# Performance work log

Hardware: AMD Instinct MI355X
Metric: run time of the kernel (lower is better)

Reference implementation:

```python
import math
import jax, jax.numpy as jnp
import numpy as np

K = 4          # beats_per_bar
POS_DIM = 32   # fourier pos-embed dim


def setup_inputs() -> dict:
    key = jax.random.key(0)
    k1, k2, k3 = jax.random.split(key, 3)
    B, M, D = 8, 8192, 1024
    beat_emb = jax.random.normal(k1, (B, M, D), dtype=jnp.float32)
    W = jax.random.normal(k2, (D, D + POS_DIM), dtype=jnp.float32) * 0.02  # nn.Linear weight [out, in]
    b = jax.random.normal(k3, (D,), dtype=jnp.float32) * 0.02
    return {"beat_emb": beat_emb, "W": W, "b": b}


def _fourier_features(pos, dim):
    # pos: [Mb] in [0,1] -> [Mb, dim] (dim even, so no zero-pad branch needed)
    half = dim // 2
    freqs = jnp.exp(jnp.linspace(0.0, math.log(1000.0), half)).astype(pos.dtype)
    ang = pos[:, None] * freqs  # [Mb, half]
    return jnp.concatenate([jnp.sin(ang), jnp.cos(ang)], axis=-1)


def reference(beat_emb, W, b):
    B, M, D = beat_emb.shape
    Mb = (M + K - 1) // K
    pad = Mb * K - M
    x = jnp.pad(beat_emb, ((0, 0), (0, pad), (0, 0))) if pad else beat_emb
    # fused segment mean: [B, Mb, K, D] -> sum -> divide by actual segment length
    sums = x.reshape(B, Mb, K, D).sum(axis=2)
    counts = jnp.minimum(K, M - jnp.arange(Mb) * K).astype(beat_emb.dtype)  # [Mb]
    out = sums / counts[None, :, None]  # [B, Mb, D]
    # fourier positional features on normalized bar index (same for every batch row)
    idx = jnp.arange(Mb, dtype=beat_emb.dtype)
    pos = jnp.clip(idx / max(1, Mb - 1), 0.0, 1.0)
    ff = _fourier_features(pos, POS_DIM)                     # [Mb, POS_DIM]
    ff = jnp.broadcast_to(ff[None], (B, Mb, POS_DIM))
    h = jnp.concatenate([out, ff], axis=-1)                  # [B, Mb, D+POS_DIM]
    return jnp.einsum('bmi,oi->bmo', h, W) + b               # Linear: x @ W.T + b
```

## Files before the change

### kernel.cpp

```cpp
#include <hip/hip_runtime.h>
#include <math.h>
#include <stdint.h>
#include <stddef.h>

typedef short bf16x8 __attribute__((ext_vector_type(8)));
typedef short bf16x4 __attribute__((ext_vector_type(4)));
typedef float f32x4  __attribute__((ext_vector_type(4)));

#define BATCH   8
#define M_IN    8192
#define D_IN    1024
#define POSD    32
#define KD      1056
#define MBARS   2048
#define MROWS   16384
#define NOUT    1024

__device__ __forceinline__ short f2bf(float f) {
    unsigned u = __builtin_bit_cast(unsigned, f);
    u += 0x7fffu + ((u >> 16) & 1u);
    return (short)(u >> 16);
}

__device__ __forceinline__ void async_load16(const short* g, short* l) {
    __builtin_amdgcn_global_load_lds((__attribute__((address_space(1))) void*)g,
                                     (__attribute__((address_space(3))) void*)l,
                                     16, 0, 0);
}

__global__ __launch_bounds__(256) void wcast(const float* __restrict__ W,
                                             short* __restrict__ Wb) {
    int i = blockIdx.x * 256 + threadIdx.x;
    float4 v = ((const float4*)W)[i];
    bf16x4 o = { f2bf(v.x), f2bf(v.y), f2bf(v.z), f2bf(v.w) };
    ((bf16x4*)Wb)[i] = o;
}

__global__ __launch_bounds__(256) void pool_ff(const float* __restrict__ x,
                                               short* __restrict__ h) {
    const int row = blockIdx.x;
    const int t   = threadIdx.x;
    const float4* src = (const float4*)(x + (size_t)row * 4096);
    float4 s0 = src[t];
    float4 s1 = src[t + 256];
    float4 s2 = src[t + 512];
    float4 s3 = src[t + 768];
    float mx = (s0.x + s1.x + s2.x + s3.x) * 0.25f;
    float my = (s0.y + s1.y + s2.y + s3.y) * 0.25f;
    float mz = (s0.z + s1.z + s2.z + s3.z) * 0.25f;
    float mw = (s0.w + s1.w + s2.w + s3.w) * 0.25f;
    bf16x4 o = { f2bf(mx), f2bf(my), f2bf(mz), f2bf(mw) };
    *(bf16x4*)(h + (size_t)row * KD + t * 4) = o;

    if (t < POSD) {
        const int mb = row & (MBARS - 1);
        float pos = (float)mb * (1.0f / (float)(MBARS - 1));
        float fr  = expf((float)(t & 15) * (6.907755278982137f / 15.0f));
        float ang = pos * fr;
        float v   = (t < 16) ? sinf(ang) : cosf(ang);
        h[(size_t)row * KD + D_IN + t] = f2bf(v);
    }
}

__global__ __launch_bounds__(256) void gemm_bt(const short* __restrict__ A,
                                               const short* __restrict__ B,
                                               const float* __restrict__ bias,
                                               float* __restrict__ C) {
    __shared__ short As[128 * 32];
    __shared__ short Bs[128 * 32];

    const int tid  = threadIdx.x;
    const int wave = tid >> 6;
    const int lane = tid & 63;
    const int wrow = wave >> 1;
    const int wcol = wave & 1;

    const int m0 = blockIdx.x * 128;
    const int n0 = blockIdx.y * 128;

    const int srow = tid >> 2;
    const int scol = (tid & 3) << 3;
    const short* ag = A + (size_t)(m0 + srow) * KD + scol;
    const short* bg = B + (size_t)(n0 + srow) * KD + scol;
    short* al = As + wave * (16 * 32);
    short* bl = Bs + wave * (16 * 32);

    const int foff = ((lane & 15) << 5) + ((lane >> 4) << 3);
    const short* afrag = As + wrow * (64 * 32) + foff;
    const short* bfrag = Bs + wcol * (64 * 32) + foff;

    f32x4 acc[4][4] = {};

    for (int k0 = 0; k0 < KD; k0 += 32) {
        __syncthreads();
        async_load16(ag + k0,            al);
        async_load16(ag + k0 + 64 * KD,  al + 64 * 32);
        async_load16(bg + k0,            bl);
        async_load16(bg + k0 + 64 * KD,  bl + 64 * 32);
        __syncthreads();

        bf16x8 a[4], b[4];
#pragma unroll
        for (int i = 0; i < 4; ++i) {
            a[i] = *(const bf16x8*)(afrag + i * (16 * 32));
            b[i] = *(const bf16x8*)(bfrag + i * (16 * 32));
        }
#pragma unroll
        for (int i = 0; i < 4; ++i)
#pragma unroll
            for (int j = 0; j < 4; ++j)
                acc[i][j] = __builtin_amdgcn_mfma_f32_16x16x32_bf16(a[i], b[j], acc[i][j], 0, 0, 0);
    }

    const int r0 = m0 + wrow * 64 + ((lane >> 4) << 2);
    const int c0 = n0 + wcol * 64 + (lane & 15);
#pragma unroll
    for (int j = 0; j < 4; ++j) {
        const int col = c0 + j * 16;
        const float bv = bias[col];
#pragma unroll
        for (int i = 0; i < 4; ++i) {
            float* cp = C + (size_t)(r0 + i * 16) * NOUT + col;
#pragma unroll
            for (int r = 0; r < 4; ++r)
                cp[(size_t)r * NOUT] = acc[i][j][r] + bv;
        }
    }
}

extern "C" void kernel_launch(void* const* d_in, const int* in_sizes, int n_in,
                              void* d_out, int out_size, void* d_ws, size_t ws_size,
                              hipStream_t stream) {
    const float* x    = (const float*)d_in[0];
    const float* W    = (const float*)d_in[1];
    const float* bias = (const float*)d_in[2];
    float* out = (float*)d_out;

    short* Wb = (short*)d_ws;
    short* h  = (short*)((char*)d_ws + (size_t)NOUT * KD * sizeof(short));

    wcast  <<<dim3(KD), dim3(256), 0, stream>>>(W, Wb);
    pool_ff<<<dim3(MROWS), dim3(256), 0, stream>>>(x, h);
    gemm_bt<<<dim3(MROWS / 128, NOUT / 128), dim3(256), 0, stream>>>(h, Wb, bias, out);
}
```

Measured before the change: 464.4 us.

## Merge prep kernels, pad K to 1088, use BK=64 with XOR-swizzled LDS

```diff
diff --git a/kernel.cpp b/kernel.cpp
--- a/kernel.cpp
+++ b/kernel.cpp
@@ -8,10 +8,10 @@
 typedef float f32x4  __attribute__((ext_vector_type(4)));
 
 #define BATCH   8
-#define M_IN    8192
 #define D_IN    1024
 #define POSD    32
 #define KD      1056
+#define KP      1088
 #define MBARS   2048
 #define MROWS   16384
 #define NOUT    1024
@@ -28,37 +28,42 @@
                                      16, 0, 0);
 }
 
-__global__ __launch_bounds__(256) void wcast(const float* __restrict__ W,
-                                             short* __restrict__ Wb) {
-    int i = blockIdx.x * 256 + threadIdx.x;
-    float4 v = ((const float4*)W)[i];
-    bf16x4 o = { f2bf(v.x), f2bf(v.y), f2bf(v.z), f2bf(v.w) };
-    ((bf16x4*)Wb)[i] = o;
-}
-
-__global__ __launch_bounds__(256) void pool_ff(const float* __restrict__ x,
-                                               short* __restrict__ h) {
-    const int row = blockIdx.x;
-    const int t   = threadIdx.x;
-    const float4* src = (const float4*)(x + (size_t)row * 4096);
-    float4 s0 = src[t];
-    float4 s1 = src[t + 256];
-    float4 s2 = src[t + 512];
-    float4 s3 = src[t + 768];
-    float mx = (s0.x + s1.x + s2.x + s3.x) * 0.25f;
-    float my = (s0.y + s1.y + s2.y + s3.y) * 0.25f;
-    float mz = (s0.z + s1.z + s2.z + s3.z) * 0.25f;
-    float mw = (s0.w + s1.w + s2.w + s3.w) * 0.25f;
-    bf16x4 o = { f2bf(mx), f2bf(my), f2bf(mz), f2bf(mw) };
-    *(bf16x4*)(h + (size_t)row * KD + t * 4) = o;
-
-    if (t < POSD) {
-        const int mb = row & (MBARS - 1);
-        float pos = (float)mb * (1.0f / (float)(MBARS - 1));
-        float fr  = expf((float)(t & 15) * (6.907755278982137f / 15.0f));
-        float ang = pos * fr;
-        float v   = (t < 16) ? sinf(ang) : cosf(ang);
-        h[(size_t)row * KD + D_IN + t] = f2bf(v);
+__global__ __launch_bounds__(256) void prep(const float* __restrict__ x,
+                                            const float* __restrict__ W,
+                                            short* __restrict__ h,
+                                            short* __restrict__ Wb) {
+    const int t = threadIdx.x;
+    const int bid = blockIdx.x;
+    if (bid < MROWS) {
+        const float4* src = (const float4*)(x + (size_t)bid * 4096);
+        float4 s0 = src[t], s1 = src[t + 256], s2 = src[t + 512], s3 = src[t + 768];
+        bf16x4 o = { f2bf((s0.x + s1.x + s2.x + s3.x) * 0.25f),
+                     f2bf((s0.y + s1.y + s2.y + s3.y) * 0.25f),
+                     f2bf((s0.z + s1.z + s2.z + s3.z) * 0.25f),
+                     f2bf((s0.w + s1.w + s2.w + s3.w) * 0.25f) };
+        short* hr = h + (size_t)bid * KP;
+        *(bf16x4*)(hr + t * 4) = o;
+        if (t < POSD) {
+            const int mb = bid & (MBARS - 1);
+            float pos = (float)mb * (1.0f / (float)(MBARS - 1));
+            float fr  = expf((float)(t & 15) * (6.907755278982137f / 15.0f));
+            float ang = pos * fr;
+            hr[D_IN + t] = f2bf((t < 16) ? sinf(ang) : cosf(ang));
+            hr[KD + t]   = 0;
+        }
+    } else {
+        const int r = bid - MROWS;
+        const float* wr = W + (size_t)r * KD;
+        short* br = Wb + (size_t)r * KP;
+        float4 v = *(const float4*)(wr + t * 4);
+        bf16x4 o = { f2bf(v.x), f2bf(v.y), f2bf(v.z), f2bf(v.w) };
+        *(bf16x4*)(br + t * 4) = o;
+        if (t < 8) {
+            float4 u = *(const float4*)(wr + 1024 + t * 4);
+            bf16x4 p = { f2bf(u.x), f2bf(u.y), f2bf(u.z), f2bf(u.w) };
+            *(bf16x4*)(br + 1024 + t * 4) = p;
+            *(bf16x4*)(br + KD + t * 4)   = (bf16x4){0, 0, 0, 0};
+        }
     }
 }
 
@@ -66,8 +71,8 @@
                                                const short* __restrict__ B,
                                                const float* __restrict__ bias,
                                                float* __restrict__ C) {
-    __shared__ short As[128 * 32];
-    __shared__ short Bs[128 * 32];
+    __shared__ short As[128 * 64];
+    __shared__ short Bs[128 * 64];
 
     const int tid  = threadIdx.x;
     const int wave = tid >> 6;
@@ -78,54 +83,63 @@
     const int m0 = blockIdx.x * 128;
     const int n0 = blockIdx.y * 128;
 
-    const int srow = tid >> 2;
-    const int scol = (tid & 3) << 3;
-    const short* ag = A + (size_t)(m0 + srow) * KD + scol;
-    const short* bg = B + (size_t)(n0 + srow) * KD + scol;
-    short* al = As + wave * (16 * 32);
-    short* bl = Bs + wave * (16 * 32);
+    const int r8   = tid >> 3;
+    const int soct = (tid & 7) ^ (r8 & 7);
+    const short* ag = A + (size_t)(m0 + r8) * KP + soct * 8;
+    const short* bg = B + (size_t)(n0 + r8) * KP + soct * 8;
+    short* al = As + wave * 512;
+    short* bl = Bs + wave * 512;
 
-    const int foff = ((lane & 15) << 5) + ((lane >> 4) << 3);
-    const short* afrag = As + wrow * (64 * 32) + foff;
-    const short* bfrag = Bs + wcol * (64 * 32) + foff;
+    const int r  = lane & 15;
+    const int q  = lane >> 4;
+    const int rx = r & 7;
+    const short* afr = As + (wrow * 64 + r) * 64;
+    const short* bfr = Bs + (wcol * 64 + r) * 64;
+    const int sl0 = ((q    ) ^ rx) * 8;
+    const int sl1 = ((4 + q) ^ rx) * 8;
 
     f32x4 acc[4][4] = {};
 
-    for (int k0 = 0; k0 < KD; k0 += 32) {
+    for (int k0 = 0; k0 < KP; k0 += 64) {
         __syncthreads();
-        async_load16(ag + k0,            al);
-        async_load16(ag + k0 + 64 * KD,  al + 64 * 32);
-        async_load16(bg + k0,            bl);
-        async_load16(bg + k0 + 64 * KD,  bl + 64 * 32);
+#pragma unroll
+        for (int i = 0; i < 4; ++i) {
+            async_load16(ag + k0 + (size_t)i * 32 * KP, al + i * 2048);
+            async_load16(bg + k0 + (size_t)i * 32 * KP, bl + i * 2048);
+        }
         __syncthreads();
 
-        bf16x8 a[4], b[4];
 #pragma unroll
-        for (int i = 0; i < 4; ++i) {
-            a[i] = *(const bf16x8*)(afrag + i * (16 * 32));
-            b[i] = *(const bf16x8*)(bfrag + i * (16 * 32));
+        for (int s = 0; s < 2; ++s) {
+            const int sl = s ? sl1 : sl0;
+            bf16x8 a[4], b[4];
+#pragma unroll
+            for (int i = 0; i < 4; ++i) {
+                a[i] = *(const bf16x8*)(afr + i * 1024 + sl);
+                b[i] = *(const bf16x8*)(bfr + i * 1024 + sl);
+            }
+#pragma unroll
+            for (int i = 0; i < 4; ++i)
+#pragma unroll
+                for (int j = 0; j < 4; ++j)
+                    acc[i][j] = __builtin_amdgcn_mfma_f32_16x16x32_bf16(a[i], b[j], acc[i][j], 0, 0, 0);
         }
+    }
+
+    const int rr0 = m0 + wrow * 64 + (q << 2);
+    const int c0  = n0 + wcol * 64 + r;
+    float bv[4];
 #pragma unroll
-        for (int i = 0; i < 4; ++i)
+    for (int j = 0; j < 4; ++j) bv[j] = bias[c0 + j * 16];
+#pragma unroll
+    for (int i = 0; i < 4; ++i)
+#pragma unroll
+        for (int rg = 0; rg < 4; ++rg) {
+            float* cp = C + (size_t)(rr0 + i * 16 + rg) * NOUT;
 #pragma unroll
             for (int j = 0; j < 4; ++j)
-                acc[i][j] = __builtin_amdgcn_mfma_f32_16x16x32_bf16(a[i], b[j], acc[i][j], 0, 0, 0);
-    }
-
-    const int r0 = m0 + wrow * 64 + ((lane >> 4) << 2);
-    const int c0 = n0 + wcol * 64 + (lane & 15);
-#pragma unroll
-    for (int j = 0; j < 4; ++j) {
-        const int col = c0 + j * 16;
-        const float bv = bias[col];
-#pragma unroll
-        for (int i = 0; i < 4; ++i) {
-            float* cp = C + (size_t)(r0 + i * 16) * NOUT + col;
-#pragma unroll
-            for (int r = 0; r < 4; ++r)
-                cp[(size_t)r * NOUT] = acc[i][j][r] + bv;
+                cp[c0 + j * 16] = acc[i][j][rg] + bv[j];
         }
-    }
 }
 
 extern "C" void kernel_launch(void* const* d_in, const int* in_sizes, int n_in,
@@ -137,9 +151,8 @@
     float* out = (float*)d_out;
 
     short* Wb = (short*)d_ws;
-    short* h  = (short*)((char*)d_ws + (size_t)NOUT * KD * sizeof(short));
+    short* h  = (short*)((char*)d_ws + (size_t)NOUT * KP * sizeof(short));
 
-    wcast  <<<dim3(KD), dim3(256), 0, stream>>>(W, Wb);
-    pool_ff<<<dim3(MROWS), dim3(256), 0, stream>>>(x, h);
+    prep   <<<dim3(MROWS + NOUT), dim3(256), 0, stream>>>(x, W, h, Wb);
     gemm_bt<<<dim3(MROWS / 128, NOUT / 128), dim3(256), 0, stream>>>(h, Wb, bias, out);
 }
```

Result: faster. 423.1 us (-8.9%).
